# Kernel tuning notes

Hardware: AMD Instinct MI355X
Metric: run time of the kernel (lower is better)

Reference implementation:

```python
import jax, jax.numpy as jnp
import numpy as np

T, K, D = 65536, 2048, 256


def setup_inputs() -> dict:
    key = jax.random.key(0)
    k1, k2 = jax.random.split(key)
    x_td = jax.random.normal(k1, (T, D), dtype=jnp.float32)
    # codebook initialized like build(): uniform in [-1/K, 1/K]; use normal-free uniform
    embeddings_kd = jax.random.uniform(k2, (K, D), minval=-1.0 / K, maxval=1.0 / K, dtype=jnp.float32)
    return {"x_td": x_td, "embeddings_kd": embeddings_kd}


def reference(x_td, embeddings_kd):
    x_sq_t = jnp.sum(x_td ** 2, axis=-1, keepdims=True)          # (T, 1)
    e_sq_k = jnp.sum(embeddings_kd ** 2, axis=-1)                # (K,)
    cross_tk = x_td @ embeddings_kd.T                            # (T, K)
    dist_tk = x_sq_t - 2.0 * cross_tk + e_sq_k                   # (T, K)
    indices_t = jnp.argmin(dist_tk, axis=-1)                     # (T,)
    # decode: gather codebook rows
    quantized_td = embeddings_kd[indices_t]                      # (T, D)
    # straight-through estimator
    quantized_td = x_td + jax.lax.stop_gradient(quantized_td - x_td)
    return quantized_td, indices_t
```

## Files before the change

kernel.cpp:

```cpp
#include <hip/hip_runtime.h>

#define T_SZ 65536
#define K_SZ 2048
#define D_SZ 256

typedef unsigned short u16;
typedef _Float16 f16;
typedef f16 f16x8 __attribute__((ext_vector_type(8)));
typedef float f32x4 __attribute__((ext_vector_type(4)));

#define RINGCAP 1024

#define GLOAD_LDS16(g, l)                                                  \
  __builtin_amdgcn_global_load_lds(                                        \
      (const __attribute__((address_space(1))) unsigned int*)(g),          \
      (__attribute__((address_space(3))) unsigned int*)(l), 16, 0, 0)

__device__ __forceinline__ int swz4(int r) { return (r & 3) ^ ((r >> 2) & 3); }

__device__ __forceinline__ float pairwise128_sq_v4(const float4* __restrict__ a4) {
#pragma clang fp contract(off)
  float4 va = a4[0], vb = a4[1];
  float r0 = va.x * va.x, r1 = va.y * va.y, r2 = va.z * va.z, r3 = va.w * va.w;
  float r4 = vb.x * vb.x, r5 = vb.y * vb.y, r6 = vb.z * vb.z, r7 = vb.w * vb.w;
#pragma unroll
  for (int i = 2; i < 32; i += 2) {
    float4 c = a4[i], d = a4[i + 1];
    r0 += c.x * c.x;
    r1 += c.y * c.y;
    r2 += c.z * c.z;
    r3 += c.w * c.w;
    r4 += d.x * d.x;
    r5 += d.y * d.y;
    r6 += d.z * d.z;
    r7 += d.w * d.w;
  }
  return ((r0 + r1) + (r2 + r3)) + ((r4 + r5) + (r6 + r7));
}

__device__ __forceinline__ float2 pairwise128_sq_abs_v4(const float4* __restrict__ a4) {
#pragma clang fp contract(off)
  float4 va = a4[0], vb = a4[1];
  float r0 = va.x * va.x, r1 = va.y * va.y, r2 = va.z * va.z, r3 = va.w * va.w;
  float r4 = vb.x * vb.x, r5 = vb.y * vb.y, r6 = vb.z * vb.z, r7 = vb.w * vb.w;
  float s0 = fabsf(va.x) + fabsf(va.y), s1 = fabsf(va.z) + fabsf(va.w);
  float s2 = fabsf(vb.x) + fabsf(vb.y), s3 = fabsf(vb.z) + fabsf(vb.w);
#pragma unroll
  for (int i = 2; i < 32; i += 2) {
    float4 c = a4[i], d = a4[i + 1];
    r0 += c.x * c.x;
    r1 += c.y * c.y;
    r2 += c.z * c.z;
    r3 += c.w * c.w;
    r4 += d.x * d.x;
    r5 += d.y * d.y;
    r6 += d.z * d.z;
    r7 += d.w * d.w;
    s0 += fabsf(c.x) + fabsf(c.y);
    s1 += fabsf(c.z) + fabsf(c.w);
    s2 += fabsf(d.x) + fabsf(d.y);
    s3 += fabsf(d.z) + fabsf(d.w);
  }
  float2 res;
  res.x = ((r0 + r1) + (r2 + r3)) + ((r4 + r5) + (r6 + r7));
  res.y = (s0 + s1) + (s2 + s3);
  return res;
}

__global__ void esq_kernel(const float* __restrict__ e, float* __restrict__ esq) {
  int k = blockIdx.x * 64 + threadIdx.x;
  const float4* er = reinterpret_cast<const float4*>(e + (size_t)k * D_SZ);
  esq[k] = pairwise128_sq_v4(er) + pairwise128_sq_v4(er + 32);
}

__global__ __launch_bounds__(256) void conv_e_kernel(const float* __restrict__ src,
                                                     u16* __restrict__ dst) {
  const int tile = blockIdx.x, tid = threadIdx.x;
  const float4* s4 = reinterpret_cast<const float4*>(src);
  u16* dt = dst + (size_t)tile * 32768;
#pragma unroll 1
  for (int it = 0; it < 16; ++it) {
    int idx = tid + it * 256;
    int G = idx & 3, row = (idx >> 2) & 127, step = idx >> 9;
    int srow = tile * 128 + row;
    int kb = step * 32 + 8 * (G ^ swz4(row));
    float4 a = s4[srow * 64 + (kb >> 2)];
    float4 b = s4[srow * 64 + (kb >> 2) + 1];
    float v[8] = {a.x, a.y, a.z, a.w, b.x, b.y, b.z, b.w};
    union { f16 h[8]; uint4 vec; } pk;
#pragma unroll
    for (int j = 0; j < 8; ++j) pk.h[j] = (f16)v[j];
    *reinterpret_cast<uint4*>(dt + (size_t)step * 4096 + row * 32 + G * 8) = pk.vec;
  }
}

__global__ __launch_bounds__(256) void conv_x_kernel(const float* __restrict__ src,
                                                     u16* __restrict__ dst) {
  const int tile = blockIdx.x, tid = threadIdx.x;
  const float4* s4 = reinterpret_cast<const float4*>(src);
  u16* dt = dst + (size_t)tile * 32768;
#pragma unroll 1
  for (int it = 0; it < 8; ++it) {
    int idx = tid + it * 256;
    int G = idx & 3, row = (idx >> 2) & 63, step = idx >> 8;
    int srow = tile * 64 + row;
    int kb = step * 32 + 8 * (G ^ swz4(row));
    float4 a = s4[srow * 64 + (kb >> 2)];
    float4 b = s4[srow * 64 + (kb >> 2) + 1];
    float v[8] = {a.x, a.y, a.z, a.w, b.x, b.y, b.z, b.w};
    union { f16 h[8]; uint4 vec; } pk;
#pragma unroll
    for (int j = 0; j < 8; ++j) pk.h[j] = (f16)v[j];
    *reinterpret_cast<uint4*>(dt + (size_t)step * 2048 + row * 32 + G * 8) = pk.vec;
  }
}

__device__ __forceinline__ float exact_cross(const float4* __restrict__ x4,
                                             const float4* __restrict__ e4,
                                             int grow, int code) {
  const float4* xr = x4 + (size_t)grow * 64;
  const float4* er = e4 + (size_t)code * 64;
  float acc = 0.0f;
#pragma unroll 8
  for (int t = 0; t < 64; ++t) {
    float4 a = xr[t], b = er[t];
    acc = __builtin_fmaf(a.x, b.x, acc);
    acc = __builtin_fmaf(a.y, b.y, acc);
    acc = __builtin_fmaf(a.z, b.z, acc);
    acc = __builtin_fmaf(a.w, b.w, acc);
  }
  return acc;
}

__global__ __launch_bounds__(256, 4) void vq_mfma_kernel(
    const float* __restrict__ x, const float* __restrict__ e,
    const u16* __restrict__ Xh, const u16* __restrict__ Eh,
    const float* __restrict__ esq_g, float* __restrict__ out,
    float* __restrict__ outIdx) {
  __shared__ __align__(16) u16 As[8][64][32];
  __shared__ float xsq_s[64], th_s[64];
  __shared__ unsigned rm1_u[64];
  __shared__ unsigned ring[RINGCAP];
  __shared__ unsigned long long ebest[64];
  __shared__ int fidx[64];
  __shared__ unsigned ringcnt;

  const int tid = threadIdx.x;
  const int lane = tid & 63;
  const int wid = tid >> 6;
  const int wm = wid >> 1, wn = wid & 1;
  const int rowbase = blockIdx.x * 64;

  if (tid == 0) ringcnt = 0;
  if (tid < 64) {
    ebest[tid] = ~0ull;
    rm1_u[tid] = 0x7F7FFFFFu;
  }

  const u16* Atile = Xh + (size_t)blockIdx.x * 32768;
  u16* AsF = &As[0][0][0];
#pragma unroll
  for (int r = 0; r < 8; ++r)
    GLOAD_LDS16(Atile + r * 2048 + wid * 512 + lane * 8, AsF + r * 2048 + wid * 512);

  const float4* x4 = reinterpret_cast<const float4*>(x);
  if (tid < 64) {
    const float4* xr = x4 + (size_t)(rowbase + tid) * 64;
    float2 p0 = pairwise128_sq_abs_v4(xr);
    float2 p1 = pairwise128_sq_abs_v4(xr + 32);
    xsq_s[tid] = p0.x + p1.x;
    th_s[tid] = 4.0e-6f * (p0.y + p1.y) + 4.0e-4f;
  }

  int offA[2], offB[4];
#pragma unroll
  for (int mf = 0; mf < 2; ++mf) {
    const int row = wm * 32 + mf * 16 + (lane & 15);
    offA[mf] = row * 32 + (((lane >> 4) ^ swz4(row)) * 8);
  }
#pragma unroll
  for (int nf = 0; nf < 4; ++nf) {
    const int cl = wn * 64 + nf * 16 + (lane & 15);
    offB[nf] = cl * 32 + (((lane >> 4) ^ swz4(cl)) * 8);
  }

  f32x4 acc[2][4];
#pragma unroll
  for (int mf = 0; mf < 2; ++mf)
#pragma unroll
    for (int nf = 0; nf < 4; ++nf) acc[mf][nf] = (f32x4){0.f, 0.f, 0.f, 0.f};

  asm volatile("s_waitcnt vmcnt(0)");
  __syncthreads();

#pragma unroll 1
  for (int chunk = 0; chunk < 16; ++chunk) {
    float esq_c[4];
#pragma unroll
    for (int nf = 0; nf < 4; ++nf)
      esq_c[nf] = esq_g[chunk * 128 + wn * 64 + nf * 16 + (lane & 15)];
    const u16* Bch = Eh + (size_t)chunk * 32768;
#pragma unroll
    for (int ks = 0; ks < 8; ++ks) {
      const u16* bg = Bch + ks * 4096;
      const u16* aa = &As[ks][0][0];
      f16x8 afr[2], bfr[4];
#pragma unroll
      for (int nf = 0; nf < 4; ++nf)
        bfr[nf] = *reinterpret_cast<const f16x8*>(bg + offB[nf]);
#pragma unroll
      for (int mf = 0; mf < 2; ++mf)
        afr[mf] = *reinterpret_cast<const f16x8*>(aa + offA[mf]);
#pragma unroll
      for (int mf = 0; mf < 2; ++mf)
#pragma unroll
        for (int nf = 0; nf < 4; ++nf)
          acc[mf][nf] = __builtin_amdgcn_mfma_f32_16x16x32_f16(
              afr[mf], bfr[nf], acc[mf][nf], 0, 0, 0);
    }
#pragma unroll
    for (int mf = 0; mf < 2; ++mf) {
#pragma unroll
      for (int rg = 0; rg < 4; ++rg) {
        const int row = wm * 32 + mf * 16 + (lane >> 4) * 4 + rg;
        const float xq = xsq_s[row];
        float dmin = 3.4e38f;
#pragma unroll
        for (int nf = 0; nf < 4; ++nf)
          dmin = fminf(dmin, (xq - 2.0f * acc[mf][nf][rg]) + esq_c[nf]);
        dmin = fminf(dmin, __shfl_xor(dmin, 1, 64));
        dmin = fminf(dmin, __shfl_xor(dmin, 2, 64));
        dmin = fminf(dmin, __shfl_xor(dmin, 4, 64));
        dmin = fminf(dmin, __shfl_xor(dmin, 8, 64));
        if ((lane & 15) == 0) atomicMin(&rm1_u[row], __float_as_uint(dmin));
      }
    }
    __syncthreads();
    const int cbase = chunk * 128 + wn * 64;
#pragma unroll
    for (int mf = 0; mf < 2; ++mf) {
#pragma unroll
      for (int rg = 0; rg < 4; ++rg) {
        const int row = wm * 32 + mf * 16 + (lane >> 4) * 4 + rg;
        const float xq = xsq_s[row];
        const float gate = __uint_as_float(rm1_u[row]) + th_s[row];
#pragma unroll
        for (int nf = 0; nf < 4; ++nf) {
          const float dv = (xq - 2.0f * acc[mf][nf][rg]) + esq_c[nf];
          if (dv <= gate) {
            unsigned slot = atomicAdd(&ringcnt, 1u);
            if (slot < RINGCAP)
              ring[slot] = ((unsigned)row << 11) |
                           (unsigned)(cbase + nf * 16 + (lane & 15));
          }
          acc[mf][nf][rg] = 0.0f;
        }
      }
    }
    __syncthreads();
  }

  const float4* e4 = reinterpret_cast<const float4*>(e);
  const unsigned cnt = ringcnt;
  if (cnt <= RINGCAP) {
    for (unsigned i = tid; i < cnt; i += 256) {
      const unsigned ent = ring[i];
      const int row = (int)(ent >> 11), code = (int)(ent & 2047u);
      const float cr = exact_cross(x4, e4, rowbase + row, code);
      const float d = (xsq_s[row] - 2.0f * cr) + esq_g[code];
      const unsigned long long key =
          (((unsigned long long)__float_as_uint(d)) << 32) | (unsigned)code;
      atomicMin(&ebest[row], key);
    }
  } else {
#pragma unroll 1
    for (int row = 0; row < 64; ++row) {
      for (int code = tid; code < K_SZ; code += 256) {
        const float cr = exact_cross(x4, e4, rowbase + row, code);
        const float d = (xsq_s[row] - 2.0f * cr) + esq_g[code];
        const unsigned long long key =
            (((unsigned long long)__float_as_uint(d)) << 32) | (unsigned)code;
        atomicMin(&ebest[row], key);
      }
    }
  }
  __syncthreads();
  if (tid < 64) fidx[tid] = (int)(ebest[tid] & 2047ull);
  __syncthreads();

  float4* out4 = reinterpret_cast<float4*>(out);
#pragma unroll 1
  for (int i = tid; i < 64 * 64; i += 256) {
    const int row = i >> 6, q = i & 63;
    const int idx = fidx[row];
    float4 xv = x4[(size_t)(rowbase + row) * 64 + q];
    float4 qv = e4[(size_t)idx * 64 + q];
    float4 o;
    o.x = xv.x + (qv.x - xv.x);
    o.y = xv.y + (qv.y - xv.y);
    o.z = xv.z + (qv.z - xv.z);
    o.w = xv.w + (qv.w - xv.w);
    out4[(size_t)(rowbase + row) * 64 + q] = o;
    if (q == 0) outIdx[rowbase + row] = (float)idx;
  }
}

extern "C" void kernel_launch(void* const* d_in, const int* in_sizes, int n_in,
                              void* d_out, int out_size, void* d_ws, size_t ws_size,
                              hipStream_t stream) {
  const float* x = (const float*)d_in[0];
  const float* e = (const float*)d_in[1];
  float* out = (float*)d_out;
  float* outIdx = out + (size_t)T_SZ * D_SZ;

  float* esq = (float*)d_ws;
  u16* Eh = (u16*)(esq + K_SZ);
  u16* Xh = (u16*)out;

  conv_x_kernel<<<T_SZ / 64, 256, 0, stream>>>(x, Xh);
  conv_e_kernel<<<K_SZ / 128, 256, 0, stream>>>(e, Eh);
  esq_kernel<<<K_SZ / 64, 64, 0, stream>>>(e, esq);
  vq_mfma_kernel<<<T_SZ / 64, 256, 0, stream>>>(x, e, Xh, Eh, esq, out, outIdx);
}
```

Before: 345.0 us.

## Fuse x fp16 conversion into VQ kernel and register-prefetch codebook fragments

Drops the separate conv_x kernel. Each VQ block now reads its fp32 x tile, converts it to fp16 and writes it into the swizzled LDS layout itself. This removes the fp16 X staging write and its later re-read through global memory, plus one kernel launch. It also double-buffers the codebook B fragments in registers so the next k-step's global loads are issued before the current MFMAs, and drops the per-chunk trailing block barrier. The trade-off is more register pressure and load issue inside the main kernel.

```diff
diff --git a/kernel.cpp b/kernel.cpp
--- a/kernel.cpp
+++ b/kernel.cpp
@@ -10,11 +10,6 @@
 typedef float f32x4 __attribute__((ext_vector_type(4)));
 
 #define RINGCAP 1024
-
-#define GLOAD_LDS16(g, l)                                                  \
-  __builtin_amdgcn_global_load_lds(                                        \
-      (const __attribute__((address_space(1))) unsigned int*)(g),          \
-      (__attribute__((address_space(3))) unsigned int*)(l), 16, 0, 0)
 
 __device__ __forceinline__ int swz4(int r) { return (r & 3) ^ ((r >> 2) & 3); }
 
@@ -94,27 +89,6 @@
   }
 }
 
-__global__ __launch_bounds__(256) void conv_x_kernel(const float* __restrict__ src,
-                                                     u16* __restrict__ dst) {
-  const int tile = blockIdx.x, tid = threadIdx.x;
-  const float4* s4 = reinterpret_cast<const float4*>(src);
-  u16* dt = dst + (size_t)tile * 32768;
-#pragma unroll 1
-  for (int it = 0; it < 8; ++it) {
-    int idx = tid + it * 256;
-    int G = idx & 3, row = (idx >> 2) & 63, step = idx >> 8;
-    int srow = tile * 64 + row;
-    int kb = step * 32 + 8 * (G ^ swz4(row));
-    float4 a = s4[srow * 64 + (kb >> 2)];
-    float4 b = s4[srow * 64 + (kb >> 2) + 1];
-    float v[8] = {a.x, a.y, a.z, a.w, b.x, b.y, b.z, b.w};
-    union { f16 h[8]; uint4 vec; } pk;
-#pragma unroll
-    for (int j = 0; j < 8; ++j) pk.h[j] = (f16)v[j];
-    *reinterpret_cast<uint4*>(dt + (size_t)step * 2048 + row * 32 + G * 8) = pk.vec;
-  }
-}
-
 __device__ __forceinline__ float exact_cross(const float4* __restrict__ x4,
                                              const float4* __restrict__ e4,
                                              int grow, int code) {
@@ -134,9 +108,8 @@
 
 __global__ __launch_bounds__(256, 4) void vq_mfma_kernel(
     const float* __restrict__ x, const float* __restrict__ e,
-    const u16* __restrict__ Xh, const u16* __restrict__ Eh,
-    const float* __restrict__ esq_g, float* __restrict__ out,
-    float* __restrict__ outIdx) {
+    const u16* __restrict__ Eh, const float* __restrict__ esq_g,
+    float* __restrict__ out, float* __restrict__ outIdx) {
   __shared__ __align__(16) u16 As[8][64][32];
   __shared__ float xsq_s[64], th_s[64];
   __shared__ unsigned rm1_u[64];
@@ -147,8 +120,7 @@
 
   const int tid = threadIdx.x;
   const int lane = tid & 63;
-  const int wid = tid >> 6;
-  const int wm = wid >> 1, wn = wid & 1;
+  const int wm = (tid >> 6) >> 1, wn = (tid >> 6) & 1;
   const int rowbase = blockIdx.x * 64;
 
   if (tid == 0) ringcnt = 0;
@@ -157,13 +129,22 @@
     rm1_u[tid] = 0x7F7FFFFFu;
   }
 
-  const u16* Atile = Xh + (size_t)blockIdx.x * 32768;
-  u16* AsF = &As[0][0][0];
-#pragma unroll
-  for (int r = 0; r < 8; ++r)
-    GLOAD_LDS16(Atile + r * 2048 + wid * 512 + lane * 8, AsF + r * 2048 + wid * 512);
-
   const float4* x4 = reinterpret_cast<const float4*>(x);
+
+  const float4* xt4 = x4 + (size_t)rowbase * 64;
+#pragma unroll 2
+  for (int it = 0; it < 8; ++it) {
+    int idx = tid + it * 256;
+    int G = idx & 3, row = (idx >> 2) & 63, ks = idx >> 8;
+    int kb = ks * 32 + 8 * (G ^ swz4(row));
+    float4 a = xt4[(size_t)row * 64 + (kb >> 2)];
+    float4 b = xt4[(size_t)row * 64 + (kb >> 2) + 1];
+    union { f16 h[8]; uint4 vec; } pk;
+    pk.h[0] = (f16)a.x; pk.h[1] = (f16)a.y; pk.h[2] = (f16)a.z; pk.h[3] = (f16)a.w;
+    pk.h[4] = (f16)b.x; pk.h[5] = (f16)b.y; pk.h[6] = (f16)b.z; pk.h[7] = (f16)b.w;
+    *reinterpret_cast<uint4*>(&As[ks][row][G * 8]) = pk.vec;
+  }
+
   if (tid < 64) {
     const float4* xr = x4 + (size_t)(rowbase + tid) * 64;
     float2 p0 = pairwise128_sq_abs_v4(xr);
@@ -190,7 +171,11 @@
 #pragma unroll
     for (int nf = 0; nf < 4; ++nf) acc[mf][nf] = (f32x4){0.f, 0.f, 0.f, 0.f};
 
-  asm volatile("s_waitcnt vmcnt(0)");
+  f16x8 bpf[2][4];
+#pragma unroll
+  for (int nf = 0; nf < 4; ++nf)
+    bpf[0][nf] = *reinterpret_cast<const f16x8*>(Eh + offB[nf]);
+
   __syncthreads();
 
 #pragma unroll 1
@@ -199,15 +184,18 @@
 #pragma unroll
     for (int nf = 0; nf < 4; ++nf)
       esq_c[nf] = esq_g[chunk * 128 + wn * 64 + nf * 16 + (lane & 15)];
-    const u16* Bch = Eh + (size_t)chunk * 32768;
 #pragma unroll
     for (int ks = 0; ks < 8; ++ks) {
-      const u16* bg = Bch + ks * 4096;
+      const int par = ks & 1;
+      const int gsn = chunk * 8 + ks + 1;
+      if (gsn < 128) {
+        const u16* bg = Eh + (size_t)gsn * 4096;
+#pragma unroll
+        for (int nf = 0; nf < 4; ++nf)
+          bpf[par ^ 1][nf] = *reinterpret_cast<const f16x8*>(bg + offB[nf]);
+      }
       const u16* aa = &As[ks][0][0];
-      f16x8 afr[2], bfr[4];
-#pragma unroll
-      for (int nf = 0; nf < 4; ++nf)
-        bfr[nf] = *reinterpret_cast<const f16x8*>(bg + offB[nf]);
+      f16x8 afr[2];
 #pragma unroll
       for (int mf = 0; mf < 2; ++mf)
         afr[mf] = *reinterpret_cast<const f16x8*>(aa + offA[mf]);
@@ -216,7 +204,7 @@
 #pragma unroll
         for (int nf = 0; nf < 4; ++nf)
           acc[mf][nf] = __builtin_amdgcn_mfma_f32_16x16x32_f16(
-              afr[mf], bfr[nf], acc[mf][nf], 0, 0, 0);
+              afr[mf], bpf[par][nf], acc[mf][nf], 0, 0, 0);
     }
 #pragma unroll
     for (int mf = 0; mf < 2; ++mf) {
@@ -257,8 +245,8 @@
         }
       }
     }
-    __syncthreads();
-  }
+  }
+  __syncthreads();
 
   const float4* e4 = reinterpret_cast<const float4*>(e);
   const unsigned cnt = ringcnt;
@@ -315,10 +303,8 @@
 
   float* esq = (float*)d_ws;
   u16* Eh = (u16*)(esq + K_SZ);
-  u16* Xh = (u16*)out;
-
-  conv_x_kernel<<<T_SZ / 64, 256, 0, stream>>>(x, Xh);
+
   conv_e_kernel<<<K_SZ / 128, 256, 0, stream>>>(e, Eh);
   esq_kernel<<<K_SZ / 64, 64, 0, stream>>>(e, esq);
-  vq_mfma_kernel<<<T_SZ / 64, 256, 0, stream>>>(x, e, Xh, Eh, esq, out, outIdx);
-}
+  vq_mfma_kernel<<<T_SZ / 64, 256, 0, stream>>>(x, e, Eh, esq, out, outIdx);
+}
```

New measurement: 324.3 us. 6.0% less time.
